# Performance work log

Measured on AMD Instinct MI355X. Metric: run time of the kernel, lower is better.

Reference implementation:

```python
import jax, jax.numpy as jnp
import numpy as np

KS, KT = 3, 3  # Chebyshev order, temporal kernel


def _conv_t(x, w, b):
    # x: [B,C,T,N], w: [C_out,C_in,KT,1] -> valid conv over T
    y = jax.lax.conv_general_dilated(x, w, (1, 1), 'VALID',
                                     dimension_numbers=('NCHW', 'OIHW', 'NCHW'))
    return y + b[None, :, None, None]


def _glu_tconv(x, w, b, aw, ab):
    c_out = w.shape[0] // 2
    # Align (c_in > c_out): 1x1 conv, then crop first KT-1 steps
    x_in = (jnp.einsum('bctn,oc->botn', x, aw) + ab[None, :, None, None])[:, :, KT - 1:, :]
    xc = _conv_t(x, w, b)
    return (xc[:, :c_out] + x_in) * jax.nn.sigmoid(xc[:, c_out:])


def _relu_tconv(x, w, b):
    c_out = w.shape[0]
    pad = c_out - x.shape[1]
    # Align (c_in < c_out): zero-pad channels, then crop first KT-1 steps
    x_in = jnp.pad(x, ((0, 0), (0, pad), (0, 0), (0, 0)))[:, :, KT - 1:, :]
    return jax.nn.relu(_conv_t(x, w, b) + x_in)


def _sconv(x, basis, theta, bias):
    # Chebyshev graph conv: knm,bitm -> bitkn then channel mix iok,bitkn -> botn
    x_c = jnp.einsum('knm,bitm->bitkn', basis, x)
    x_gc = jnp.einsum('iok,bitkn->botn', theta, x_c) + bias[None, :, None, None]
    return jax.nn.relu(x_gc + x)  # align is identity (c_in == c_out)


def _layer_norm(x, g, b):
    # LayerNorm over [node_num, channels]: permute to [B,T,N,C], normalize last 2 dims
    y = jnp.transpose(x, (0, 2, 3, 1))
    mu = jnp.mean(y, axis=(-2, -1), keepdims=True)
    var = jnp.var(y, axis=(-2, -1), keepdims=True)
    y = (y - mu) * jax.lax.rsqrt(var + 1e-5) * g + b
    return jnp.transpose(y, (0, 3, 1, 2))


def _cheb_basis(graph):
    n = graph.shape[0]
    eye = jnp.eye(n, dtype=graph.dtype)
    g = graph + eye
    d = jnp.clip(jnp.sum(g, axis=-1), 1e-6, None) ** -0.5
    lap = eye - d[:, None] * g * d[None, :]
    cheb = [eye, lap]
    for _ in range(2, KS):
        cheb.append(2.0 * (lap @ cheb[-1]) - cheb[-2])
    return jnp.stack(cheb[:KS])


def _block(x, basis, t1_w, t1_b, t1_aw, t1_ab, s_theta, s_bias, t2_w, t2_b, ln_g, ln_b):
    x = _glu_tconv(x, t1_w, t1_b, t1_aw, t1_ab)
    x = _sconv(x, basis, s_theta, s_bias)
    x = _relu_tconv(x, t2_w, t2_b)
    return _layer_norm(x, ln_g, ln_b)  # dropout: eval mode (identity)


def setup_inputs() -> dict:
    B, N, T = 16, 2000, 12
    D_IN, D_OUT, C_MID = 3, 64, 32
    keys = jax.random.split(jax.random.key(0), 24)
    k = iter(range(24))

    def nrm(shape, scale=0.05):
        return jax.random.normal(keys[next(k)], shape, dtype=jnp.float32) * scale

    inp = {}
    inp['x'] = jax.random.normal(keys[next(k)], (B, D_IN, T, N), dtype=jnp.float32)
    inp['graph'] = jax.random.uniform(keys[next(k)], (N, N), dtype=jnp.float32)
    inp['in_w'] = nrm((D_IN, D_OUT), 0.3)
    inp['in_b'] = nrm((D_OUT,))
    for blk in ('b1', 'b2'):
        inp[blk + '_t1_w'] = nrm((2 * C_MID, D_OUT, KT, 1))
        inp[blk + '_t1_b'] = nrm((2 * C_MID,))
        inp[blk + '_t1_aw'] = nrm((C_MID, D_OUT))
        inp[blk + '_t1_ab'] = nrm((C_MID,))
        inp[blk + '_s_theta'] = nrm((C_MID, C_MID, KS))
        inp[blk + '_s_bias'] = nrm((C_MID,))
        inp[blk + '_t2_w'] = nrm((D_OUT, C_MID, KT, 1))
        inp[blk + '_t2_b'] = nrm((D_OUT,))
        inp[blk + '_ln_g'] = jnp.ones((N, D_OUT), dtype=jnp.float32)
        inp[blk + '_ln_b'] = jnp.zeros((N, D_OUT), dtype=jnp.float32)
    return inp


def reference(x, graph, in_w, in_b,
              b1_t1_w, b1_t1_b, b1_t1_aw, b1_t1_ab, b1_s_theta, b1_s_bias,
              b1_t2_w, b1_t2_b, b1_ln_g, b1_ln_b,
              b2_t1_w, b2_t1_b, b2_t1_aw, b2_t1_ab, b2_s_theta, b2_s_bias,
              b2_t2_w, b2_t2_b, b2_ln_g, b2_ln_b):
    # input_conv: 1x1 conv == channel matmul
    h = jnp.einsum('bctn,co->botn', x, in_w) + in_b[None, :, None, None]
    basis = _cheb_basis(graph)
    h = _block(h, basis, b1_t1_w, b1_t1_b, b1_t1_aw, b1_t1_ab,
               b1_s_theta, b1_s_bias, b1_t2_w, b1_t2_b, b1_ln_g, b1_ln_b)
    h = _block(h, basis, b2_t1_w, b2_t1_b, b2_t1_aw, b2_t1_ab,
               b2_s_theta, b2_s_bias, b2_t2_w, b2_t2_b, b2_ln_g, b2_ln_b)
    return h  # [B, 64, T-4*(KT-1)=4, N]
```

## Files before the change

### kernel.cpp

```cpp
#include <hip/hip_runtime.h>


typedef unsigned short u16;
typedef __attribute__((ext_vector_type(8))) short short8;
typedef __attribute__((ext_vector_type(4))) float floatx4;

struct __attribute__((aligned(8))) us4 { u16 v[4]; };

#define AS1 __attribute__((address_space(1)))
#define AS3 __attribute__((address_space(3)))

__device__ __forceinline__ float b2f(u16 h) {
  union { unsigned int u; float f; } v;
  v.u = ((unsigned int)h) << 16;
  return v.f;
}
__device__ __forceinline__ u16 f2b(float f) {
  union { float f; unsigned int u; } v;
  v.f = f;
  unsigned int r = (v.u + 0x7fffu + ((v.u >> 16) & 1u)) >> 16;
  return (u16)r;
}
__device__ __forceinline__ void gl_lds16(const u16* g, u16* l) {
  __builtin_amdgcn_global_load_lds((const AS1 unsigned int*)g,
                                   (AS3 unsigned int*)l, 16, 0, 0);
}
__device__ __forceinline__ us4 load4_guard(const u16* gp, int n) {
  if (n + 3 < 2000) return *(const us4*)gp;
  us4 r;
#pragma unroll
  for (int i = 0; i < 4; ++i) r.v[i] = (n + i < 2000) ? gp[i] : (u16)0;
  return r;
}


__global__ void k_deg(const float* __restrict__ graph, float* __restrict__ d) {
  const int n = blockIdx.x;
  const int tid = threadIdx.x;
  float s = 0.f;
  const float* row = graph + (size_t)n * 2000;
  for (int m4 = tid; m4 < 500; m4 += 256) {
    const float4 g = *(const float4*)(row + m4 * 4);
    s += (g.x + g.y) + (g.z + g.w);
  }
  __shared__ float red[256];
  red[tid] = s;
  __syncthreads();
  for (int st = 128; st > 0; st >>= 1) {
    if (tid < st) red[tid] += red[tid + st];
    __syncthreads();
  }
  if (tid == 0) d[n] = rsqrtf(fmaxf(red[0] + 1.f, 1e-6f));
}

__global__ void k_lap(const float* __restrict__ graph, const float* __restrict__ d,
                      u16* __restrict__ L) {
  const int m = blockIdx.x * 1024 + threadIdx.x * 4;
  const int n = blockIdx.y;
  us4 r = {{0, 0, 0, 0}};
  if (n < 2000 && m < 2000) {
    const float4 g4 = *(const float4*)(graph + (size_t)n * 2000 + m);
    const float4 d4 = *(const float4*)(d + m);
    const float dn = d[n];
    const float gv[4] = {g4.x, g4.y, g4.z, g4.w};
    const float dv[4] = {d4.x, d4.y, d4.z, d4.w};
#pragma unroll
    for (int i = 0; i < 4; ++i) {
      const float delta = (n == m + i) ? 1.f : 0.f;
      r.v[i] = f2b(delta - dn * (gv[i] + delta) * dv[i]);
    }
  }
  *(us4*)(L + (size_t)n * 2048 + m) = r;
}


__global__ void k_inconv(const float* __restrict__ x, const float* __restrict__ w,
                         const float* __restrict__ bias, u16* __restrict__ h0) {
  const int n = blockIdx.x * 1024 + threadIdx.x * 4;
  if (n >= 2000) return;
  const int b = blockIdx.y / 12, t = blockIdx.y % 12;
  const float4 x0 = *(const float4*)(x + ((size_t)(b * 3 + 0) * 12 + t) * 2000 + n);
  const float4 x1 = *(const float4*)(x + ((size_t)(b * 3 + 1) * 12 + t) * 2000 + n);
  const float4 x2 = *(const float4*)(x + ((size_t)(b * 3 + 2) * 12 + t) * 2000 + n);
  for (int o = 0; o < 64; ++o) {
    const float w0 = w[o], w1 = w[64 + o], w2 = w[128 + o], bb = bias[o];
    us4 r;
    r.v[0] = f2b(x0.x * w0 + x1.x * w1 + x2.x * w2 + bb);
    r.v[1] = f2b(x0.y * w0 + x1.y * w1 + x2.y * w2 + bb);
    r.v[2] = f2b(x0.z * w0 + x1.z * w1 + x2.z * w2 + bb);
    r.v[3] = f2b(x0.w * w0 + x1.w * w1 + x2.w * w2 + bb);
    *(us4*)(h0 + ((size_t)(b * 64 + o) * 12 + t) * 2000 + n) = r;
  }
}

__global__ void k_wpack(const float* __restrict__ t1w, const float* __restrict__ aw,
                        const float* __restrict__ th, const float* __restrict__ t2w,
                        u16* __restrict__ wglu, u16* __restrict__ wth,
                        u16* __restrict__ wt2) {
  const int mode = blockIdx.x;
  const int tid = threadIdx.x;
  if (mode == 0) {
    for (int idx = tid; idx < 1536 * 8; idx += 256) {
      int chunk = idx >> 3, j = idx & 7;
      int l15 = chunk & 15, quad = (chunk >> 4) & 3, g = chunk >> 6;
      int ks = g % 6, mi = g / 6;
      int o = mi * 16 + l15;
      int k = ks * 32 + quad * 8 + j;
      int c = k & 63, dt = k >> 6;
      float v = t1w[(o * 64 + c) * 3 + dt];
      if (o < 32 && dt == 2) v += aw[o * 64 + c];
      wglu[idx] = f2b(v);
    }
  } else if (mode == 1) {
    for (int idx = tid; idx < 512 * 8; idx += 256) {
      int chunk = idx >> 3, j = idx & 7;
      int l15 = chunk & 15, quad = (chunk >> 4) & 3, g = chunk >> 6;
      float v = 0.f;
      if (g < 6) {
        int ks = g % 3, mi = g / 3;
        int o = mi * 16 + l15;
        int k = ks * 32 + quad * 8 + j;
        int i = k & 31, src = k >> 5;
        const float* p = th + (i * 32 + o) * 3;
        v = (src == 0) ? (p[0] - p[2]) : (src == 1 ? p[1] : 2.f * p[2]);
      }
      wth[idx] = f2b(v);
    }
  } else {
    for (int idx = tid; idx < 768 * 8; idx += 256) {
      int chunk = idx >> 3, j = idx & 7;
      int l15 = chunk & 15, quad = (chunk >> 4) & 3, g = chunk >> 6;
      int ks = g % 3, mi = g / 3;
      int o = mi * 16 + l15;
      int k = ks * 32 + quad * 8 + j;
      int i = k & 31, dt = k >> 5;
      wt2[idx] = f2b(t2w[(o * 32 + i) * 3 + dt]);
    }
  }
}

template <int MODE>
__global__ __launch_bounds__(256, 3)
void k_mix(const u16* __restrict__ x0, const u16* __restrict__ wp,
           const float* __restrict__ b0, const float* __restrict__ b1,
           u16* __restrict__ out, int T_in, int T) {
  constexpr int K = 192;
  constexpr int KS = K / 32;
  constexpr int MT = 4;
  constexpr int NT = 64;
  constexpr int NBLK = NT / 16;
  constexpr int TPR = NT / 4;
  constexpr int GPP = 256 / TPR;
  constexpr int WCH = ((MT * KS * 64) + 255) & ~255;
  constexpr int XCH = KS * NBLK * 65;
  __shared__ __align__(16) u16 lw[WCH * 8];
  __shared__ __align__(16) u16 lx[XCH * 8];

  const int tid = threadIdx.x;
  const int lane = tid & 63, wave = tid >> 6;
  const int quad = lane >> 4, l15 = lane & 15;
  const int n0 = blockIdx.x * NT;
  const int b = blockIdx.y / T, t = blockIdx.y % T;

#pragma unroll
  for (int p = 0; p < WCH / 256; ++p)
    gl_lds16(wp + (size_t)(p * 256 + wave * 64 + lane) * 8,
             &lw[(p * 256 + wave * 64) * 8]);

  const bool guard = (n0 + NT > 2000);
  const int nloc = (tid % TPR) * 4;
  us4 rv[3][4];
#pragma unroll
  for (int p = 0; p < 3; ++p) {
    const int k4 = p * GPP + (tid / TPR);
#pragma unroll
    for (int i = 0; i < 4; ++i) {
      const int k = k4 * 4 + i;
      const u16* rp =
          x0 + (size_t)((b * 64 + (k & 63)) * T_in + t + (k >> 6)) * 2000;
      rv[p][i] = guard ? load4_guard(rp + n0 + nloc, n0 + nloc)
                       : *(const us4*)(rp + n0 + nloc);
    }
  }
#pragma unroll
  for (int p = 0; p < 3; ++p) {
    const int k4 = p * GPP + (tid / TPR);
    const int ks = k4 >> 3, q8 = k4 & 7;
    const int quadw = (q8 >> 1) & 3;
    const int j0 = (q8 & 1) * 4;
#pragma unroll
    for (int i = 0; i < 4; ++i) {
      const int nn = nloc + i;
      const int chunk = (ks * NBLK + (nn >> 4)) * 65 + quadw * 16 + (nn & 15);
      us4 wv;
      wv.v[0] = rv[p][0].v[i]; wv.v[1] = rv[p][1].v[i];
      wv.v[2] = rv[p][2].v[i]; wv.v[3] = rv[p][3].v[i];
      *(us4*)&lx[chunk * 8 + j0] = wv;
    }
  }
  asm volatile("s_waitcnt vmcnt(0)" ::: "memory");
  __syncthreads();

  floatx4 acc[MT] = {};
#pragma unroll
  for (int ks = 0; ks < KS; ++ks) {
    short8 bfr = *(const short8*)&lx[(((ks * NBLK + wave) * 65) + lane) * 8];
#pragma unroll
    for (int mi = 0; mi < MT; ++mi) {
      short8 afr = *(const short8*)&lw[((mi * KS + ks) * 64 + lane) * 8];
      acc[mi] = __builtin_amdgcn_mfma_f32_16x16x32_bf16(afr, bfr, acc[mi], 0, 0, 0);
    }
  }

  const int n = n0 + wave * 16 + l15;
#pragma unroll
  for (int mi = 0; mi < 2; ++mi)
#pragma unroll
    for (int r = 0; r < 4; ++r) {
      const int i = mi * 16 + quad * 4 + r;
      const float sv = acc[mi][r] + b0[i] + b1[i];
      const float gt = acc[mi + 2][r] + b0[32 + i];
      const float val = sv / (1.f + __expf(-gt));
      out[(size_t)((b * 32 + i) * T + t) * 2048 + n] = f2b(val);
    }
}

__global__ __launch_bounds__(256, 2)
void k_mix12(const u16* __restrict__ x0, const u16* __restrict__ y1,
             const u16* __restrict__ y2, const u16* __restrict__ wth,
             const u16* __restrict__ wt2, const float* __restrict__ sb,
             const float* __restrict__ t2b, u16* __restrict__ out,
             int T_g, int T_o) {
  __shared__ __align__(16) u16 lw1[512 * 8];
  __shared__ __align__(16) u16 lw2[768 * 8];
  __shared__ __align__(16) u16 lx[780 * 8];
  __shared__ __align__(16) u16 lt[10 * 260 * 8];

  const int tid = threadIdx.x;
  const int lane = tid & 63, wave = tid >> 6;
  const int quad = lane >> 4, l15 = lane & 15;
  const int n0 = blockIdx.x * 64;
  const int b = blockIdx.y;
  const int n = n0 + wave * 16 + l15;

#pragma unroll
  for (int p = 0; p < 2; ++p)
    gl_lds16(wth + (size_t)(p * 256 + wave * 64 + lane) * 8,
             &lw1[(p * 256 + wave * 64) * 8]);
#pragma unroll
  for (int p = 0; p < 3; ++p)
    gl_lds16(wt2 + (size_t)(p * 256 + wave * 64 + lane) * 8,
             &lw2[(p * 256 + wave * 64) * 8]);

  const int nloc = (tid & 15) * 4;
  const int g16 = tid >> 4;

  for (int t = 0; t < T_g; ++t) {
    __syncthreads();
    us4 rv[2][4];
#pragma unroll
    for (int p = 0; p < 2; ++p) {
      const int k4 = p * 16 + g16;
      if (k4 < 24) {
#pragma unroll
        for (int i = 0; i < 4; ++i) {
          const int k = k4 * 4 + i;
          const u16* base = (k < 32) ? x0 : ((k < 64) ? y1 : y2);
          rv[p][i] = *(const us4*)(base +
              (size_t)((b * 32 + (k & 31)) * T_g + t) * 2048 + n0 + nloc);
        }
      }
    }
#pragma unroll
    for (int p = 0; p < 2; ++p) {
      const int k4 = p * 16 + g16;
      if (k4 < 24) {
        const int ks = k4 >> 3, q8 = k4 & 7;
        const int quadw = (q8 >> 1) & 3;
        const int j0 = (q8 & 1) * 4;
#pragma unroll
        for (int i = 0; i < 4; ++i) {
          const int nn = nloc + i;
          const int chunk = (ks * 4 + (nn >> 4)) * 65 + quadw * 16 + (nn & 15);
          us4 wv;
          wv.v[0] = rv[p][0].v[i]; wv.v[1] = rv[p][1].v[i];
          wv.v[2] = rv[p][2].v[i]; wv.v[3] = rv[p][3].v[i];
          *(us4*)&lx[chunk * 8 + j0] = wv;
        }
      }
    }
    __syncthreads();

    floatx4 acc[2] = {};
#pragma unroll
    for (int ks = 0; ks < 3; ++ks) {
      short8 bfr = *(const short8*)&lx[((ks * 4 + wave) * 65 + lane) * 8];
#pragma unroll
      for (int mi = 0; mi < 2; ++mi) {
        short8 afr = *(const short8*)&lw1[((mi * 3 + ks) * 64 + lane) * 8];
        acc[mi] = __builtin_amdgcn_mfma_f32_16x16x32_bf16(afr, bfr, acc[mi], 0, 0, 0);
      }
    }
#pragma unroll
    for (int mi = 0; mi < 2; ++mi)
#pragma unroll
      for (int r = 0; r < 4; ++r) {
        const int o = mi * 16 + quad * 4 + r;
        const float v = acc[mi][r] + sb[o] +
            b2f(lx[(wave * 65 + ((o >> 3) & 3) * 16 + l15) * 8 + (o & 7)]);
        lt[((t * 4 + wave) * 65 + ((o >> 3) & 3) * 16 + l15) * 8 + (o & 7)] =
            f2b(fmaxf(v, 0.f));
      }
  }
  __syncthreads();

  for (int to = 0; to < T_o; ++to) {
    floatx4 acc[4] = {};
#pragma unroll
    for (int ks = 0; ks < 3; ++ks) {
      short8 bfr = *(const short8*)&lt[(((to + ks) * 4 + wave) * 65 + lane) * 8];
#pragma unroll
      for (int mi = 0; mi < 4; ++mi) {
        short8 afr = *(const short8*)&lw2[((mi * 3 + ks) * 64 + lane) * 8];
        acc[mi] = __builtin_amdgcn_mfma_f32_16x16x32_bf16(afr, bfr, acc[mi], 0, 0, 0);
      }
    }
    if (n < 2000) {
#pragma unroll
      for (int mi = 0; mi < 4; ++mi)
#pragma unroll
        for (int r = 0; r < 4; ++r) {
          const int o = mi * 16 + quad * 4 + r;
          float v = acc[mi][r] + t2b[o];
          if (o < 32)
            v += b2f(lt[(((to + 2) * 4 + wave) * 65 +
                         ((o >> 3) & 3) * 16 + l15) * 8 + (o & 7)]);
          out[(size_t)((b * 64 + o) * T_o + to) * 2000 + n] = f2b(fmaxf(v, 0.f));
        }
    }
  }
}

template <int BM, int MPAD, int DPW>
__global__ __launch_bounds__(512, 1)
void k_gemm(const u16* __restrict__ A, const u16* __restrict__ Bt,
            u16* __restrict__ C) {
  constexpr int K = 2048;
  constexpr int NTI = K / 64;
  constexpr int AFR = BM / 32;
  constexpr int WM = BM / 2;
  constexpr int S1 = (AFR + 1) / 2;
  constexpr int C1 = DPW - 4;
  constexpr int BROWS = 512;
  constexpr int ROWS = BROWS + 2 * MPAD;
  __shared__ __align__(16) u16 lds[2][ROWS * 32];

  const int tid = threadIdx.x;
  const int lane = tid & 63, wave = tid >> 6;
  const int quad = lane >> 4, l15 = lane & 15;
  const int m0 = blockIdx.y * BM, n0 = blockIdx.x * 256;
  const int wy = wave >> 2, wx = wave & 3;

  const int lr = lane >> 2;
  const int qv = (((lane & 3) - (lr + (lr >> 2))) & 3);
  const u16* sp[DPW];
  int dofs[DPW];
#pragma unroll
  for (int d = 0; d < DPW; ++d) {
    const int f = wave * DPW + d;
    if (f < 32) {
      const int rb = f >> 1, ks = f & 1;
      sp[d] = Bt + (size_t)(n0 + rb * 16 + lr) * K + ks * 32 + qv * 8;
      dofs[d] = (ks * 256 + rb * 16) * 32;
    } else {
      const int g = f - 32;
      const int rb = g >> 1, ks = g & 1;
      sp[d] = A + (size_t)(m0 + rb * 16 + lr) * K + ks * 32 + qv * 8;
      dofs[d] = (BROWS + ks * MPAD + rb * 16) * 32;
    }
  }

  const int sigr = (l15 + (l15 >> 2)) & 3;
  const int cofs = ((quad + sigr) & 3) * 8;

  floatx4 acc[AFR][4] = {};

#pragma unroll
  for (int d = 0; d < DPW; ++d) gl_lds16(sp[d], &lds[0][dofs[d]]);
#pragma unroll
  for (int d = 0; d < C1; ++d) gl_lds16(sp[d] + 64, &lds[1][dofs[d]]);
  if constexpr (C1 == 3) asm volatile("s_waitcnt vmcnt(3)" ::: "memory");
  else                   asm volatile("s_waitcnt vmcnt(2)" ::: "memory");
  asm volatile("s_barrier" ::: "memory");

  for (int it = 0; it < NTI; ++it) {
    const u16* cb = lds[it & 1];
    u16* nb = lds[(it & 1) ^ 1];
    u16* pb = lds[it & 1];
    const int kn1 = (it + 1) * 64;
    const bool st1 = (it + 1 < NTI);
    short8 bf[4], af[AFR];

#pragma unroll
    for (int ni = 0; ni < 4; ++ni)
      bf[ni] = *(const short8*)&cb[(wx * 64 + ni * 16 + l15) * 32 + cofs];
#pragma unroll
    for (int mi = 0; mi < S1; ++mi)
      af[mi] = *(const short8*)&cb[(BROWS + wy * WM + mi * 16 + l15) * 32 + cofs];
    if (st1) {
      gl_lds16(sp[C1] + kn1, &nb[dofs[C1]]);
      gl_lds16(sp[C1 + 1] + kn1, &nb[dofs[C1 + 1]]);
    }
#pragma unroll
    for (int mi = 0; mi < S1; ++mi)
#pragma unroll
      for (int ni = 0; ni < 4; ++ni)
        acc[mi][ni] = __builtin_amdgcn_mfma_f32_16x16x32_bf16(
            af[mi], bf[ni], acc[mi][ni], 0, 0, 0);

#pragma unroll
    for (int mi = S1; mi < AFR; ++mi)
      af[mi] = *(const short8*)&cb[(BROWS + wy * WM + mi * 16 + l15) * 32 + cofs];
    if (st1) {
      gl_lds16(sp[C1 + 2] + kn1, &nb[dofs[C1 + 2]]);
      gl_lds16(sp[C1 + 3] + kn1, &nb[dofs[C1 + 3]]);
    }
#pragma unroll
    for (int mi = S1; mi < AFR; ++mi)
#pragma unroll
      for (int ni = 0; ni < 4; ++ni)
        acc[mi][ni] = __builtin_amdgcn_mfma_f32_16x16x32_bf16(
            af[mi], bf[ni], acc[mi][ni], 0, 0, 0);

#pragma unroll
    for (int ni = 0; ni < 4; ++ni)
      bf[ni] = *(const short8*)&cb[(256 + wx * 64 + ni * 16 + l15) * 32 + cofs];
#pragma unroll
    for (int mi = 0; mi < S1; ++mi)
      af[mi] = *(const short8*)&cb[(BROWS + MPAD + wy * WM + mi * 16 + l15) * 32 + cofs];
#pragma unroll
    for (int mi = 0; mi < S1; ++mi)
#pragma unroll
      for (int ni = 0; ni < 4; ++ni)
        acc[mi][ni] = __builtin_amdgcn_mfma_f32_16x16x32_bf16(
            af[mi], bf[ni], acc[mi][ni], 0, 0, 0);

#pragma unroll
    for (int mi = S1; mi < AFR; ++mi)
      af[mi] = *(const short8*)&cb[(BROWS + MPAD + wy * WM + mi * 16 + l15) * 32 + cofs];
#pragma unroll
    for (int mi = S1; mi < AFR; ++mi)
#pragma unroll
      for (int ni = 0; ni < 4; ++ni)
        acc[mi][ni] = __builtin_amdgcn_mfma_f32_16x16x32_bf16(
            af[mi], bf[ni], acc[mi][ni], 0, 0, 0);

    asm volatile("s_waitcnt lgkmcnt(0)" ::: "memory");
    asm volatile("s_barrier" ::: "memory");
    if (it + 2 < NTI) {
      const int kn2 = (it + 2) * 64;
#pragma unroll
      for (int d = 0; d < C1; ++d) gl_lds16(sp[d] + kn2, &pb[dofs[d]]);
      if constexpr (C1 == 3) asm volatile("s_waitcnt vmcnt(3)" ::: "memory");
      else                   asm volatile("s_waitcnt vmcnt(2)" ::: "memory");
    } else {
      asm volatile("s_waitcnt vmcnt(0)" ::: "memory");
    }
    asm volatile("s_barrier" ::: "memory");
  }

#pragma unroll
  for (int mi = 0; mi < AFR; ++mi) {
#pragma unroll
    for (int ni = 0; ni < 4; ++ni) {
      const int row = m0 + wy * WM + mi * 16 + quad * 4;
      const int col = n0 + wx * 64 + ni * 16 + l15;
#pragma unroll
      for (int r = 0; r < 4; ++r)
        C[(size_t)(row + r) * K + col] = f2b(acc[mi][ni][r]);
    }
  }
}


__global__ void k_lnpart(const u16* __restrict__ h, float* __restrict__ part, int T) {
  const int bt = blockIdx.x, cg = blockIdx.y;
  const int b = bt / T, t = bt % T;
  const int tid = threadIdx.x;
  float s = 0.f, ss = 0.f;
  for (int c = cg * 8; c < cg * 8 + 8; ++c) {
    const u16* row = h + (size_t)((b * 64 + c) * T + t) * 2000;
    for (int n = tid * 4; n < 2000; n += 1024) {
      const us4 hv = *(const us4*)(row + n);
#pragma unroll
      for (int i = 0; i < 4; ++i) {
        const float v = b2f(hv.v[i]);
        s += v; ss += v * v;
      }
    }
  }
  __shared__ float r1[256], r2[256];
  r1[tid] = s; r2[tid] = ss;
  __syncthreads();
  for (int st = 128; st > 0; st >>= 1) {
    if (tid < st) { r1[tid] += r1[tid + st]; r2[tid] += r2[tid + st]; }
    __syncthreads();
  }
  if (tid == 0) {
    part[(bt * 8 + cg) * 2 + 0] = r1[0];
    part[(bt * 8 + cg) * 2 + 1] = r2[0];
  }
}

__global__ void k_lnfin(const float* __restrict__ part, float* __restrict__ stats,
                        int BT) {
  const int i = blockIdx.x * 256 + threadIdx.x;
  if (i >= BT) return;
  float s = 0.f, ss = 0.f;
  for (int g = 0; g < 8; ++g) {
    s  += part[(i * 8 + g) * 2 + 0];
    ss += part[(i * 8 + g) * 2 + 1];
  }
  const float inv = 1.f / 128000.f;
  const float mu = s * inv;
  const float var = ss * inv - mu * mu;
  stats[i * 2] = mu;
  stats[i * 2 + 1] = rsqrtf(var + 1e-5f);
}

__global__ void k_lngbT(const float* __restrict__ gw, const float* __restrict__ gb,
                        float* __restrict__ gwT, float* __restrict__ gbT) {
  const int n = blockIdx.x * 256 + threadIdx.x;
  const int c = blockIdx.y;
  float vw = 0.f, vb = 0.f;
  if (n < 2000) {
    vw = gw[(size_t)n * 64 + c];
    vb = gb[(size_t)n * 64 + c];
  }
  gwT[(size_t)c * 2048 + n] = vw;
  gbT[(size_t)c * 2048 + n] = vb;
}

__global__ void k_lnapply(u16* __restrict__ h, const float* __restrict__ stats,
                          const float* __restrict__ gwT, const float* __restrict__ gbT,
                          float* __restrict__ outf, int T, int write_f32) {
  const int n = blockIdx.x * 1024 + threadIdx.x * 4;
  if (n >= 2000) return;
  int by = blockIdx.y;
  const int t = by % T; by /= T;
  const int c = by & 63;
  const int b = by >> 6;
  const int bt = b * T + t;
  const float mu = stats[bt * 2], rs = stats[bt * 2 + 1];
  const size_t row = (size_t)((b * 64 + c) * T + t) * 2000 + n;
  const us4 hv = *(const us4*)(h + row);
  const float4 w4 = *(const float4*)(gwT + (size_t)c * 2048 + n);
  const float4 b4 = *(const float4*)(gbT + (size_t)c * 2048 + n);
  const float o0 = (b2f(hv.v[0]) - mu) * rs * w4.x + b4.x;
  const float o1 = (b2f(hv.v[1]) - mu) * rs * w4.y + b4.y;
  const float o2 = (b2f(hv.v[2]) - mu) * rs * w4.z + b4.z;
  const float o3 = (b2f(hv.v[3]) - mu) * rs * w4.w + b4.w;
  if (write_f32) {
    *(float4*)(outf + row) = make_float4(o0, o1, o2, o3);
  } else {
    us4 r;
    r.v[0] = f2b(o0); r.v[1] = f2b(o1); r.v[2] = f2b(o2); r.v[3] = f2b(o3);
    *(us4*)(h + row) = r;
  }
}


extern "C" void kernel_launch(void* const* d_in, const int* in_sizes, int n_in,
                              void* d_out, int out_size, void* d_ws, size_t ws_size,
                              hipStream_t stream) {
  const float* x     = (const float*)d_in[0];
  const float* graph = (const float*)d_in[1];
  const float* in_w  = (const float*)d_in[2];
  const float* in_b  = (const float*)d_in[3];

  char* ws = (char*)d_ws;
  size_t off = 0;
  auto alloc = [&](size_t bytes) -> void* {
    void* p = ws + off;
    off += (bytes + 255) & ~(size_t)255;
    return p;
  };
  float* dd    = (float*)alloc(2048 * 4);
  float* stats = (float*)alloc(16 * 12 * 2 * 4);
  float* part  = (float*)alloc(16 * 8 * 8 * 2 * 4);
  float* gwT   = (float*)alloc((size_t)64 * 2048 * 4);
  float* gbT   = (float*)alloc((size_t)64 * 2048 * 4);
  u16* wpg  = (u16*)alloc((size_t)1536 * 8 * 2);
  u16* wpt  = (u16*)alloc((size_t)512 * 8 * 2);
  u16* wp2  = (u16*)alloc((size_t)768 * 8 * 2);
  u16* L    = (u16*)alloc((size_t)2048 * 2048 * 2);
  u16* h0   = (u16*)alloc((size_t)16 * 64 * 12 * 2000 * 2);
  u16* Xp   = (u16*)alloc((size_t)5120 * 2048 * 2);
  u16* Y1   = (u16*)alloc((size_t)5120 * 2048 * 2);
  u16* Y2   = (u16*)alloc((size_t)5120 * 2048 * 2);
  u16* h1   = (u16*)alloc((size_t)16 * 64 * 8 * 2000 * 2);
  u16* h2   = h0;
  if (off > ws_size) return;

  k_deg<<<dim3(2000), dim3(256), 0, stream>>>(graph, dd);
  k_lap<<<dim3(2, 2048), dim3(256), 0, stream>>>(graph, dd, L);
  k_inconv<<<dim3(2, 192), dim3(256), 0, stream>>>(x, in_w, in_b, h0);

  for (int blk = 0; blk < 2; ++blk) {
    const int base = 4 + blk * 10;
    const float* t1w = (const float*)d_in[base + 0];
    const float* t1b = (const float*)d_in[base + 1];
    const float* aw  = (const float*)d_in[base + 2];
    const float* ab  = (const float*)d_in[base + 3];
    const float* th  = (const float*)d_in[base + 4];
    const float* sb  = (const float*)d_in[base + 5];
    const float* t2w = (const float*)d_in[base + 6];
    const float* t2b = (const float*)d_in[base + 7];
    const float* lng = (const float*)d_in[base + 8];
    const float* lnb = (const float*)d_in[base + 9];

    const int T_in = (blk == 0) ? 12 : 8;
    const int T_g  = T_in - 2;
    const int T_o  = T_g - 2;
    const u16* hin = (blk == 0) ? h0 : h1;
    u16* hout      = (blk == 0) ? h1 : h2;

    k_wpack<<<dim3(3), dim3(256), 0, stream>>>(t1w, aw, th, t2w, wpg, wpt, wp2);
    k_lngbT<<<dim3(8, 64), dim3(256), 0, stream>>>(lng, lnb, gwT, gbT);
    k_mix<0><<<dim3(32, 16 * T_g), dim3(256), 0, stream>>>(
        hin, wpg, t1b, ab, Xp, T_in, T_g);
    if (blk == 0) {
      k_gemm<160, 192, 7><<<dim3(8, 32), dim3(512), 0, stream>>>(Xp, L, Y1);
      k_gemm<160, 192, 7><<<dim3(8, 32), dim3(512), 0, stream>>>(Y1, L, Y2);
    } else {
      k_gemm<96, 128, 6><<<dim3(8, 32), dim3(512), 0, stream>>>(Xp, L, Y1);
      k_gemm<96, 128, 6><<<dim3(8, 32), dim3(512), 0, stream>>>(Y1, L, Y2);
    }
    k_mix12<<<dim3(32, 16), dim3(256), 0, stream>>>(
        Xp, Y1, Y2, wpt, wp2, sb, t2b, hout, T_g, T_o);
    k_lnpart<<<dim3(16 * T_o, 8), dim3(256), 0, stream>>>(hout, part, T_o);
    k_lnfin<<<dim3(1), dim3(256), 0, stream>>>(part, stats, 16 * T_o);
    k_lnapply<<<dim3(2, 16 * 64 * T_o), dim3(256), 0, stream>>>(
        hout, stats, gwT, gbT, (float*)d_out, T_o, blk);
  }
}
```

Baseline: 485.5 us.

## Store block inputs channel-last so GLU mix reads MFMA fragments directly

The input conv and the block-1 layernorm now write activations in a [b,t,n,c] channel-last bf16 layout padded to 2048 nodes. The GLU temporal-mix kernel can then load B fragments straight from global memory with no LDS transpose staging. Each block also loops over several time steps, reusing the weights already in LDS. The cost is a transposing layernorm-apply kernel between blocks and strided channel-last writes in the input conv.

Measured after the change: 479.8 us. No clear change (-1.2%).

```diff
diff --git a/kernel.cpp b/kernel.cpp
--- a/kernel.cpp
+++ b/kernel.cpp
@@ -73,23 +73,34 @@
   *(us4*)(L + (size_t)n * 2048 + m) = r;
 }
 
-
 __global__ void k_inconv(const float* __restrict__ x, const float* __restrict__ w,
-                         const float* __restrict__ bias, u16* __restrict__ h0) {
+                         const float* __restrict__ bias, u16* __restrict__ h0T) {
   const int n = blockIdx.x * 1024 + threadIdx.x * 4;
-  if (n >= 2000) return;
   const int b = blockIdx.y / 12, t = blockIdx.y % 12;
+  u16* op = h0T + ((size_t)(b * 12 + t) * 2048 + n) * 64;
+  if (n >= 2000) {
+    const us4 z = {{0, 0, 0, 0}};
+#pragma unroll
+    for (int i = 0; i < 64; ++i) *(us4*)(op + i * 4) = z;
+    return;
+  }
   const float4 x0 = *(const float4*)(x + ((size_t)(b * 3 + 0) * 12 + t) * 2000 + n);
   const float4 x1 = *(const float4*)(x + ((size_t)(b * 3 + 1) * 12 + t) * 2000 + n);
   const float4 x2 = *(const float4*)(x + ((size_t)(b * 3 + 2) * 12 + t) * 2000 + n);
-  for (int o = 0; o < 64; ++o) {
-    const float w0 = w[o], w1 = w[64 + o], w2 = w[128 + o], bb = bias[o];
-    us4 r;
-    r.v[0] = f2b(x0.x * w0 + x1.x * w1 + x2.x * w2 + bb);
-    r.v[1] = f2b(x0.y * w0 + x1.y * w1 + x2.y * w2 + bb);
-    r.v[2] = f2b(x0.z * w0 + x1.z * w1 + x2.z * w2 + bb);
-    r.v[3] = f2b(x0.w * w0 + x1.w * w1 + x2.w * w2 + bb);
-    *(us4*)(h0 + ((size_t)(b * 64 + o) * 12 + t) * 2000 + n) = r;
+  const float a0[4] = {x0.x, x0.y, x0.z, x0.w};
+  const float a1[4] = {x1.x, x1.y, x1.z, x1.w};
+  const float a2[4] = {x2.x, x2.y, x2.z, x2.w};
+#pragma unroll
+  for (int ni = 0; ni < 4; ++ni) {
+    for (int o4 = 0; o4 < 16; ++o4) {
+      us4 r;
+#pragma unroll
+      for (int j = 0; j < 4; ++j) {
+        const int o = o4 * 4 + j;
+        r.v[j] = f2b(a0[ni] * w[o] + a1[ni] * w[64 + o] + a2[ni] * w[128 + o] + bias[o]);
+      }
+      *(us4*)(op + ni * 64 + o4 * 4) = r;
+    }
   }
 }
 
@@ -139,90 +150,67 @@
   }
 }
 
-template <int MODE>
-__global__ __launch_bounds__(256, 3)
-void k_mix(const u16* __restrict__ x0, const u16* __restrict__ wp,
-           const float* __restrict__ b0, const float* __restrict__ b1,
-           u16* __restrict__ out, int T_in, int T) {
-  constexpr int K = 192;
-  constexpr int KS = K / 32;
-  constexpr int MT = 4;
-  constexpr int NT = 64;
-  constexpr int NBLK = NT / 16;
-  constexpr int TPR = NT / 4;
-  constexpr int GPP = 256 / TPR;
-  constexpr int WCH = ((MT * KS * 64) + 255) & ~255;
-  constexpr int XCH = KS * NBLK * 65;
-  __shared__ __align__(16) u16 lw[WCH * 8];
-  __shared__ __align__(16) u16 lx[XCH * 8];
-
+__global__ __launch_bounds__(256, 4)
+void k_mixT(const u16* __restrict__ xT, const u16* __restrict__ wp,
+            const float* __restrict__ b0, const float* __restrict__ b1,
+            u16* __restrict__ out, int T_in, int T, int tcnt) {
+  __shared__ __align__(16) u16 lw[1536 * 8];
   const int tid = threadIdx.x;
   const int lane = tid & 63, wave = tid >> 6;
   const int quad = lane >> 4, l15 = lane & 15;
-  const int n0 = blockIdx.x * NT;
-  const int b = blockIdx.y / T, t = blockIdx.y % T;
-
-#pragma unroll
-  for (int p = 0; p < WCH / 256; ++p)
+  const int n0 = blockIdx.x * 64;
+  const int b = blockIdx.y;
+  const int t0 = blockIdx.z * tcnt;
+
+#pragma unroll
+  for (int p = 0; p < 6; ++p)
     gl_lds16(wp + (size_t)(p * 256 + wave * 64 + lane) * 8,
              &lw[(p * 256 + wave * 64) * 8]);
 
-  const bool guard = (n0 + NT > 2000);
-  const int nloc = (tid % TPR) * 4;
-  us4 rv[3][4];
-#pragma unroll
-  for (int p = 0; p < 3; ++p) {
-    const int k4 = p * GPP + (tid / TPR);
-#pragma unroll
-    for (int i = 0; i < 4; ++i) {
-      const int k = k4 * 4 + i;
-      const u16* rp =
-          x0 + (size_t)((b * 64 + (k & 63)) * T_in + t + (k >> 6)) * 2000;
-      rv[p][i] = guard ? load4_guard(rp + n0 + nloc, n0 + nloc)
-                       : *(const us4*)(rp + n0 + nloc);
-    }
-  }
-#pragma unroll
-  for (int p = 0; p < 3; ++p) {
-    const int k4 = p * GPP + (tid / TPR);
-    const int ks = k4 >> 3, q8 = k4 & 7;
-    const int quadw = (q8 >> 1) & 3;
-    const int j0 = (q8 & 1) * 4;
-#pragma unroll
-    for (int i = 0; i < 4; ++i) {
-      const int nn = nloc + i;
-      const int chunk = (ks * NBLK + (nn >> 4)) * 65 + quadw * 16 + (nn & 15);
-      us4 wv;
-      wv.v[0] = rv[p][0].v[i]; wv.v[1] = rv[p][1].v[i];
-      wv.v[2] = rv[p][2].v[i]; wv.v[3] = rv[p][3].v[i];
-      *(us4*)&lx[chunk * 8 + j0] = wv;
-    }
-  }
+  float svb[8], gtb[8];
+#pragma unroll
+  for (int mi = 0; mi < 2; ++mi)
+#pragma unroll
+    for (int r = 0; r < 4; ++r) {
+      const int i = mi * 16 + quad * 4 + r;
+      svb[mi * 4 + r] = b0[i] + b1[i];
+      gtb[mi * 4 + r] = b0[32 + i];
+    }
+
+  const int n = n0 + wave * 16 + l15;
+  const u16* px = xT + ((size_t)(b * T_in + t0) * 2048 + n) * 64 + quad * 8;
+
   asm volatile("s_waitcnt vmcnt(0)" ::: "memory");
   __syncthreads();
 
-  floatx4 acc[MT] = {};
-#pragma unroll
-  for (int ks = 0; ks < KS; ++ks) {
-    short8 bfr = *(const short8*)&lx[(((ks * NBLK + wave) * 65) + lane) * 8];
-#pragma unroll
-    for (int mi = 0; mi < MT; ++mi) {
-      short8 afr = *(const short8*)&lw[((mi * KS + ks) * 64 + lane) * 8];
-      acc[mi] = __builtin_amdgcn_mfma_f32_16x16x32_bf16(afr, bfr, acc[mi], 0, 0, 0);
-    }
-  }
-
-  const int n = n0 + wave * 16 + l15;
-#pragma unroll
-  for (int mi = 0; mi < 2; ++mi)
-#pragma unroll
-    for (int r = 0; r < 4; ++r) {
-      const int i = mi * 16 + quad * 4 + r;
-      const float sv = acc[mi][r] + b0[i] + b1[i];
-      const float gt = acc[mi + 2][r] + b0[32 + i];
-      const float val = sv / (1.f + __expf(-gt));
-      out[(size_t)((b * 32 + i) * T + t) * 2048 + n] = f2b(val);
-    }
+  for (int tt = 0; tt < tcnt; ++tt) {
+    const int t = t0 + tt;
+    short8 f[6];
+#pragma unroll
+    for (int ks = 0; ks < 6; ++ks)
+      f[ks] = *(const short8*)(px + (size_t)(ks >> 1) * (2048 * 64) + (ks & 1) * 32);
+    px += 2048 * 64;
+
+    floatx4 acc[4] = {};
+#pragma unroll
+    for (int ks = 0; ks < 6; ++ks)
+#pragma unroll
+      for (int mi = 0; mi < 4; ++mi) {
+        short8 afr = *(const short8*)&lw[((mi * 6 + ks) * 64 + lane) * 8];
+        acc[mi] = __builtin_amdgcn_mfma_f32_16x16x32_bf16(afr, f[ks], acc[mi], 0, 0, 0);
+      }
+
+#pragma unroll
+    for (int mi = 0; mi < 2; ++mi)
+#pragma unroll
+      for (int r = 0; r < 4; ++r) {
+        const int i = mi * 16 + quad * 4 + r;
+        const float sv = acc[mi][r] + svb[mi * 4 + r];
+        const float gt = acc[mi + 2][r] + gtb[mi * 4 + r];
+        const float val = sv / (1.f + __expf(-gt));
+        out[(size_t)((b * 32 + i) * T + t) * 2048 + n] = f2b(val);
+      }
+  }
 }
 
 __global__ __launch_bounds__(256, 2)
@@ -528,6 +516,53 @@
   stats[i * 2 + 1] = rsqrtf(var + 1e-5f);
 }
 
+__global__ __launch_bounds__(256, 4)
+void k_lnapT(const u16* __restrict__ h, const float* __restrict__ stats,
+             const float* __restrict__ gw, const float* __restrict__ gb,
+             u16* __restrict__ hT, int T) {
+  __shared__ u16 tile[64][72];
+  const int tid = threadIdx.x;
+  const int n0 = blockIdx.x * 64;
+  const int bt = blockIdx.y;
+  const int b = bt / T, t = bt % T;
+  const float mu = stats[bt * 2], rs = stats[bt * 2 + 1];
+
+  {
+    const int c = tid >> 2;
+    const int nq = (tid & 3) * 16;
+    const u16* row = h + (size_t)((b * 64 + c) * T + t) * 2000 + n0 + nq;
+#pragma unroll
+    for (int k = 0; k < 4; ++k) {
+      const us4 v = load4_guard(row + k * 4, n0 + nq + k * 4);
+      *(us4*)&tile[c][nq + k * 4] = v;
+    }
+  }
+  __syncthreads();
+
+  const int n = tid >> 2;
+  const int c0 = (tid & 3) * 16;
+  const int gn = n0 + n;
+  u16* dst = hT + ((size_t)(b * T + t) * 2048 + gn) * 64 + c0;
+  if (gn >= 2000) {
+    const us4 z = {{0, 0, 0, 0}};
+#pragma unroll
+    for (int q = 0; q < 4; ++q) *(us4*)(dst + q * 4) = z;
+    return;
+  }
+#pragma unroll
+  for (int q = 0; q < 4; ++q) {
+    us4 r;
+#pragma unroll
+    for (int j = 0; j < 4; ++j) {
+      const int cc = c0 + q * 4 + j;
+      const float gv = gw[(size_t)gn * 64 + cc];
+      const float bv = gb[(size_t)gn * 64 + cc];
+      r.v[j] = f2b((b2f(tile[cc][n]) - mu) * rs * gv + bv);
+    }
+    *(us4*)(dst + q * 4) = r;
+  }
+}
+
 __global__ void k_lngbT(const float* __restrict__ gw, const float* __restrict__ gb,
                         float* __restrict__ gwT, float* __restrict__ gbT) {
   const int n = blockIdx.x * 256 + threadIdx.x;
@@ -541,9 +576,9 @@
   gbT[(size_t)c * 2048 + n] = vb;
 }
 
-__global__ void k_lnapply(u16* __restrict__ h, const float* __restrict__ stats,
+__global__ void k_lnapply(const u16* __restrict__ h, const float* __restrict__ stats,
                           const float* __restrict__ gwT, const float* __restrict__ gbT,
-                          float* __restrict__ outf, int T, int write_f32) {
+                          float* __restrict__ outf, int T) {
   const int n = blockIdx.x * 1024 + threadIdx.x * 4;
   if (n >= 2000) return;
   int by = blockIdx.y;
@@ -560,13 +595,7 @@
   const float o1 = (b2f(hv.v[1]) - mu) * rs * w4.y + b4.y;
   const float o2 = (b2f(hv.v[2]) - mu) * rs * w4.z + b4.z;
   const float o3 = (b2f(hv.v[3]) - mu) * rs * w4.w + b4.w;
-  if (write_f32) {
-    *(float4*)(outf + row) = make_float4(o0, o1, o2, o3);
-  } else {
-    us4 r;
-    r.v[0] = f2b(o0); r.v[1] = f2b(o1); r.v[2] = f2b(o2); r.v[3] = f2b(o3);
-    *(us4*)(h + row) = r;
-  }
+  *(float4*)(outf + row) = make_float4(o0, o1, o2, o3);
 }
 
 
@@ -594,17 +623,17 @@
   u16* wpt  = (u16*)alloc((size_t)512 * 8 * 2);
   u16* wp2  = (u16*)alloc((size_t)768 * 8 * 2);
   u16* L    = (u16*)alloc((size_t)2048 * 2048 * 2);
-  u16* h0   = (u16*)alloc((size_t)16 * 64 * 12 * 2000 * 2);
+  u16* h0T  = (u16*)alloc((size_t)16 * 12 * 2048 * 64 * 2);
   u16* Xp   = (u16*)alloc((size_t)5120 * 2048 * 2);
   u16* Y1   = (u16*)alloc((size_t)5120 * 2048 * 2);
   u16* Y2   = (u16*)alloc((size_t)5120 * 2048 * 2);
   u16* h1   = (u16*)alloc((size_t)16 * 64 * 8 * 2000 * 2);
-  u16* h2   = h0;
+  u16* h1T  = h0T;
   if (off > ws_size) return;
 
   k_deg<<<dim3(2000), dim3(256), 0, stream>>>(graph, dd);
   k_lap<<<dim3(2, 2048), dim3(256), 0, stream>>>(graph, dd, L);
-  k_inconv<<<dim3(2, 192), dim3(256), 0, stream>>>(x, in_w, in_b, h0);
+  k_inconv<<<dim3(2, 192), dim3(256), 0, stream>>>(x, in_w, in_b, h0T);
 
   for (int blk = 0; blk < 2; ++blk) {
     const int base = 4 + blk * 10;
@@ -622,13 +651,11 @@
     const int T_in = (blk == 0) ? 12 : 8;
     const int T_g  = T_in - 2;
     const int T_o  = T_g - 2;
-    const u16* hin = (blk == 0) ? h0 : h1;
-    u16* hout      = (blk == 0) ? h1 : h2;
+    const u16* hinT = (blk == 0) ? h0T : h1T;
 
     k_wpack<<<dim3(3), dim3(256), 0, stream>>>(t1w, aw, th, t2w, wpg, wpt, wp2);
-    k_lngbT<<<dim3(8, 64), dim3(256), 0, stream>>>(lng, lnb, gwT, gbT);
-    k_mix<0><<<dim3(32, 16 * T_g), dim3(256), 0, stream>>>(
-        hin, wpg, t1b, ab, Xp, T_in, T_g);
+    k_mixT<<<dim3(32, 16, 2), dim3(256), 0, stream>>>(
+        hinT, wpg, t1b, ab, Xp, T_in, T_g, T_g / 2);
     if (blk == 0) {
       k_gemm<160, 192, 7><<<dim3(8, 32), dim3(512), 0, stream>>>(Xp, L, Y1);
       k_gemm<160, 192, 7><<<dim3(8, 32), dim3(512), 0, stream>>>(Y1, L, Y2);
@@ -637,10 +664,16 @@
       k_gemm<96, 128, 6><<<dim3(8, 32), dim3(512), 0, stream>>>(Y1, L, Y2);
     }
     k_mix12<<<dim3(32, 16), dim3(256), 0, stream>>>(
-        Xp, Y1, Y2, wpt, wp2, sb, t2b, hout, T_g, T_o);
-    k_lnpart<<<dim3(16 * T_o, 8), dim3(256), 0, stream>>>(hout, part, T_o);
+        Xp, Y1, Y2, wpt, wp2, sb, t2b, h1, T_g, T_o);
+    k_lnpart<<<dim3(16 * T_o, 8), dim3(256), 0, stream>>>(h1, part, T_o);
     k_lnfin<<<dim3(1), dim3(256), 0, stream>>>(part, stats, 16 * T_o);
-    k_lnapply<<<dim3(2, 16 * 64 * T_o), dim3(256), 0, stream>>>(
-        hout, stats, gwT, gbT, (float*)d_out, T_o, blk);
-  }
-}
+    if (blk == 0) {
+      k_lnapT<<<dim3(32, 16 * T_o), dim3(256), 0, stream>>>(
+          h1, stats, lng, lnb, h1T, T_o);
+    } else {
+      k_lngbT<<<dim3(8, 64), dim3(256), 0, stream>>>(lng, lnb, gwT, gbT);
+      k_lnapply<<<dim3(2, 16 * 64 * T_o), dim3(256), 0, stream>>>(
+          h1, stats, gwT, gbT, (float*)d_out, T_o);
+    }
+  }
+}
```
